# Optimization experiments

Hardware: AMD Instinct MI355X
Metric: run time of the kernel (lower is better)

The kernel has to match this reference:

```python
import jax, jax.numpy as jnp
import numpy as np

T, B, H, OUT = 64, 4096, 256, 2
SLOPE = 25.0  # snntorch surrogate.fast_sigmoid default slope


@jax.custom_vjp
def spike(x):
    # Heaviside forward, fast-sigmoid surrogate gradient backward
    return (x > 0).astype(x.dtype)

def _spk_fwd(x):
    return (x > 0).astype(x.dtype), x

def _spk_bwd(x, g):
    return (g / (SLOPE * jnp.abs(x) + 1.0) ** 2,)

spike.defvjp(_spk_fwd, _spk_bwd)


def temporal_embedding(length):
    center = length // 2
    sigma = length / 10
    pos = np.arange(length)
    e = np.exp(-0.5 * ((pos - center) / sigma) ** 2)
    e = (e - e.min()) / (e.max() - e.min())
    return jnp.asarray(e, dtype=jnp.float32)


def setup_inputs() -> dict:
    key = jax.random.key(0)
    ks = jax.random.split(key, 16)

    def lin(k, o, i):
        bound = 1.0 / np.sqrt(i)
        kw, kb = jax.random.split(k)
        W = jax.random.uniform(kw, (o, i), minval=-bound, maxval=bound, dtype=jnp.float32)
        b = jax.random.uniform(kb, (o,), minval=-bound, maxval=bound, dtype=jnp.float32)
        return W, b

    W_in, b_in = lin(ks[0], H, 3)
    W_h, b_h = lin(ks[1], H, H)
    W_h2, b_h2 = lin(ks[2], H, H)
    W_out, b_out = lin(ks[3], OUT, H)
    W_pred, b_pred = lin(ks[4], OUT, T * 4)
    u = lambda k, n: jax.random.uniform(k, (n,), dtype=jnp.float32)
    return {
        "x": jax.random.normal(ks[5], (T, B, 3), dtype=jnp.float32),
        "W_in": W_in, "b_in": b_in,
        "beta_in": u(ks[6], H), "thr_in": u(ks[7], H),
        "W_h": W_h, "b_h": b_h,
        "beta_h": u(ks[8], H), "thr_h": u(ks[9], H),
        "W_h2": W_h2, "b_h2": b_h2,
        "beta_h2": u(ks[10], H), "thr_h2": u(ks[11], H),
        "W_out": W_out, "b_out": b_out,
        "beta_out": u(ks[12], OUT),
        "W_pred": W_pred, "b_pred": b_pred,
    }


def reference(x, W_in, b_in, beta_in, thr_in, W_h, b_h, beta_h, thr_h,
              W_h2, b_h2, beta_h2, thr_h2, W_out, b_out, beta_out,
              W_pred, b_pred):
    Tn, Bsz = x.shape[0], x.shape[1]
    emb = temporal_embedding(Tn)
    x = x * emb[:, None, None]  # per-timestep Gaussian temporal weighting

    def lif(cur, mem, beta, thr):
        # snnTorch Leaky, reset_mechanism='subtract': reset from PREVIOUS mem (detached)
        reset = jax.lax.stop_gradient((mem - thr > 0).astype(cur.dtype))
        mem = jnp.clip(beta, 0.0, 1.0) * mem + cur - reset * thr
        return spike(mem - thr), mem

    def step(carry, x_t):
        m1, m2, m4, m3 = carry
        s1, m1 = lif(x_t @ W_in.T + b_in, m1, beta_in, thr_in)
        s2, m2 = lif(s1 @ W_h.T + b_h, m2, beta_h, thr_h)
        s4, m4 = lif(s2 @ W_h2.T + b_h2, m4, beta_h2, thr_h2)
        # li_out: reset_mechanism='none', default threshold=1.0
        m3 = jnp.clip(beta_out, 0.0, 1.0) * m3 + s4 @ W_out.T + b_out
        spk_out = spike(m3 - 1.0)
        return (m1, m2, m4, m3), (spk_out, m3)

    z = lambda n: jnp.zeros((Bsz, n), x.dtype)
    init = (z(W_in.shape[0]), z(W_h.shape[0]), z(W_h2.shape[0]), z(W_out.shape[0]))
    _, (spk_rec, mem_rec) = jax.lax.scan(step, init, x)
    out = jnp.concatenate([spk_rec, mem_rec], axis=-1)  # [T, B, 2*OUT]
    # torch .view(B, T*2*OUT) on contiguous [T,B,2*OUT] == plain reshape
    out = out.reshape(Bsz, Tn * out.shape[-1])
    return out @ W_pred.T + b_pred  # [B, OUT]
```

## Files before the change

kernel.cpp:

```cpp
#include <hip/hip_runtime.h>
#include <hip/hip_bf16.h>

#define TT 64
#define BB 4096
#define HH 256
#define BMb 16
#define NBLK (BB / BMb)
#define TC 4
#define NCH (TT / TC)

typedef short bf16x8_t __attribute__((ext_vector_type(8)));
typedef float f32x4_t  __attribute__((ext_vector_type(4)));

#define WS_WA_B   0u
#define WS_EMB_B  786432u
#define WS_REC_B  1048576u

__device__ __forceinline__ float clip01f(float v) {
    return fminf(fmaxf(v, 0.0f), 1.0f);
}

__global__ __launch_bounds__(64) void setup_emb_kernel(float* __restrict__ emb) {
    int i = threadIdx.x;
    const double sigma = 64.0 / 10.0;
    const double c = 32.0;
    double d = ((double)i - c) / sigma;
    double e = exp(-0.5 * (d * d));
    double d0 = (0.0 - c) / sigma;
    double emin = exp(-0.5 * (d0 * d0));
    emb[i] = (float)((e - emin) / (1.0 - emin));
}

__global__ __launch_bounds__(256) void split_weights_kernel(
    const float* __restrict__ W_h, const float* __restrict__ W_h2,
    unsigned short* __restrict__ WA)
{
    int flat = blockIdx.x * 256 + threadIdx.x;
    int j     = flat & 7;
    int lane  = (flat >> 3) & 63;
    int c     = flat >> 9;
    int tile  = c & 1;
    int c2    = c >> 1;
    int part  = c2 % 3;
    int c3    = c2 / 3;
    int kt    = c3 & 7;
    int c4    = c3 >> 3;
    int layer = c4 & 1;
    int wv    = c4 >> 1;
    int ntile = wv * 2 + tile;
    int k = kt * 32 + (lane >> 4) * 8 + j;
    int n = ntile * 16 + (lane & 15);
    const float* W = layer ? W_h2 : W_h;
    float w = W[n * HH + k];
    __hip_bfloat16 h = __float2bfloat16(w);
    float r1 = w - __bfloat162float(h);
    __hip_bfloat16 m = __float2bfloat16(r1);
    float r2 = r1 - __bfloat162float(m);
    __hip_bfloat16 l = __float2bfloat16(r2);
    __hip_bfloat16 v = (part == 0) ? h : ((part == 1) ? m : l);
    WA[flat] = *reinterpret_cast<unsigned short*>(&v);
}

union U16x8 { uint4 u; bf16x8_t v; };


#define AS1 __attribute__((address_space(1)))
#define AS3 __attribute__((address_space(3)))
__device__ __forceinline__ void gl16(const void* g, void* l) {
    __builtin_amdgcn_global_load_lds((AS1 const void*)g, (AS3 void*)l, 16, 0, 0);
}

#define ISSUE6(Wc, ktn, sl) do {                                               \
    const char* gb_ = (const char*)(Wc) + (ktn) * 6144;                        \
    char* lb_ = myring + (sl) * 6144;                                          \
    gl16(gb_,          lb_);                                                   \
    gl16(gb_ + 1024,   lb_ + 1024);                                            \
    gl16(gb_ + 2048,   lb_ + 2048);                                            \
    gl16(gb_ + 3072,   lb_ + 3072);                                            \
    gl16(gb_ + 4096,   lb_ + 4096);                                            \
    gl16(gb_ + 5120,   lb_ + 5120);                                            \
} while (0)

#define MFMA8T(wa_, wb_, ktb) do {                                             \
    _Pragma("unroll")                                                          \
    for (int tt_ = 0; tt_ < TC; ++tt_) {                                       \
        U16x8 br_; br_.u = BfL[tt_ * 512 + (ktb) * 64];                        \
        D0[tt_] = __builtin_amdgcn_mfma_f32_16x16x32_bf16(wa_.v, br_.v, D0[tt_], 0, 0, 0); \
        D1[tt_] = __builtin_amdgcn_mfma_f32_16x16x32_bf16(wb_.v, br_.v, D1[tt_], 0, 0, 0); \
    }                                                                          \
} while (0)

#define STEPT(sl, ktb, Wi, kti) do {                                           \
    asm volatile("s_waitcnt vmcnt(6)" ::: "memory");                           \
    __builtin_amdgcn_sched_barrier(0);                                         \
    {                                                                          \
        U16x8 wa_, wb_;                                                        \
        wa_.u = ringRd[(sl) * 384 + 0];                                        \
        wb_.u = ringRd[(sl) * 384 + 64];                                       \
        MFMA8T(wa_, wb_, ktb);                                                 \
    }                                                                          \
    {                                                                          \
        U16x8 wa_, wb_;                                                        \
        wa_.u = ringRd[(sl) * 384 + 128];                                      \
        wb_.u = ringRd[(sl) * 384 + 192];                                      \
        MFMA8T(wa_, wb_, ktb);                                                 \
    }                                                                          \
    {                                                                          \
        U16x8 wa_, wb_;                                                        \
        wa_.u = ringRd[(sl) * 384 + 256];                                      \
        wb_.u = ringRd[(sl) * 384 + 320];                                      \
        asm volatile("s_waitcnt lgkmcnt(0)" ::: "memory");                     \
        __builtin_amdgcn_sched_barrier(0);                                     \
        ISSUE6(Wi, kti, sl);                                                   \
        MFMA8T(wa_, wb_, ktb);                                                 \
    }                                                                          \
} while (0)

#define GPHASE(Wc, Wn) do {                                                    \
    STEPT(0, 0, Wc, 2);                                                        \
    STEPT(1, 1, Wc, 3);                                                        \
    STEPT(0, 2, Wc, 4);                                                        \
    STEPT(1, 3, Wc, 5);                                                        \
    STEPT(0, 4, Wc, 6);                                                        \
    STEPT(1, 5, Wc, 7);                                                        \
    STEPT(0, 6, Wn, 0);                                                        \
    STEPT(1, 7, Wn, 1);                                                        \
} while (0)

__device__ __forceinline__ void compute_p(
    const float* __restrict__ WoutS, const unsigned long long (*__restrict__ M3Lt)[4],
    int wb, int ooc, float* __restrict__ pout, int lane)
{
    if (lane < 32) {
        float p = 0.f;
        for (int k = 0; k < HH; ++k) {
            int ww = k >> 4, gg = (k >> 2) & 3, reg = k & 3;
            unsigned long long word = M3Lt[ww][reg];
            unsigned w32 = (gg < 2) ? (unsigned)word : (unsigned)(word >> 32);
            int sh = ((gg & 1) << 4) | wb;
            unsigned bit = (w32 >> sh) & 1u;
            float wv = WoutS[ooc * HH + k];
            p = p + (bit ? wv : 0.f);
        }
        pout[lane] = p;
    }
}

__device__ __forceinline__ void li_walker_bits(
    const float* __restrict__ WoutS, const unsigned long long (*__restrict__ M3Lt)[4],
    int wb, int ooc, float bto, float bo, float& m3s,
    float* __restrict__ rec, int t, int b0, int lane)
{
    if (lane < 32) {
        float p = 0.f;
        for (int k = 0; k < HH; ++k) {
            int ww = k >> 4, gg = (k >> 2) & 3, reg = k & 3;
            unsigned long long word = M3Lt[ww][reg];
            unsigned w32 = (gg < 2) ? (unsigned)word : (unsigned)(word >> 32);
            int sh = ((gg & 1) << 4) | wb;
            unsigned bit = (w32 >> sh) & 1u;
            float wv = WoutS[ooc * HH + k];
            p = p + (bit ? wv : 0.f);
        }
        float mm3 = fmaf(bto, m3s, p);
        mm3 = mm3 + bo;
        m3s = mm3;
        float spk = ((m3s - 1.0f) > 0.f) ? 1.f : 0.f;
        float om3 = __shfl_xor(m3s, 16, 64);
        float osp = __shfl_xor(spk, 16, 64);
        if (lane < 16) {
            *(float4*)(rec + ((size_t)t * BB + b0 + wb) * 4) =
                make_float4(spk, osp, m3s, om3);
        }
    }
}

__global__ __launch_bounds__(512) void snn_main_kernel(
    const float* __restrict__ x,
    const float* __restrict__ W_in, const float* __restrict__ b_in,
    const float* __restrict__ beta_in, const float* __restrict__ thr_in,
    const float* __restrict__ b_h, const float* __restrict__ beta_h, const float* __restrict__ thr_h,
    const float* __restrict__ b_h2, const float* __restrict__ beta_h2, const float* __restrict__ thr_h2,
    const float* __restrict__ W_out, const float* __restrict__ b_out, const float* __restrict__ beta_out,
    const unsigned short* __restrict__ WA, const float* __restrict__ emb,
    float* __restrict__ rec)
{
#pragma clang fp contract(off)
    const int tid = threadIdx.x;
    const int w = tid >> 6;
    const int lane = tid & 63;
    const int b = lane & 15;
    const int g = lane >> 4;
    const int b0 = blockIdx.x * BMb;

    __shared__ __align__(16) unsigned short frag[TC][8 * 64 * 8];
    __shared__ unsigned long long M3L[TC][16][4];
    __shared__ float pbuf[TC][32];
    __shared__ __align__(16) float WoutS[2 * HH];
    __shared__ float4 PL1a[HH];
    __shared__ float2 PL1b[HH];
    __shared__ float4 PL2[HH];
    __shared__ float4 PL3[HH];
    __shared__ float  xs[TT][BMb][3];
    __shared__ float  embS[TT];
    __shared__ __align__(16) char ring[8 * 2 * 6144];

    char* myring = ring + w * 12288;
    const uint4* ringRd = (const uint4*)(ring + w * 12288 + lane * 16);
    const uint4* BfL = (const uint4*)frag + lane;

    WoutS[tid] = W_out[tid];
    if (tid < HH) {
        int n = tid;
        PL1a[n] = make_float4(W_in[n * 3], W_in[n * 3 + 1], W_in[n * 3 + 2], b_in[n]);
        PL1b[n] = make_float2(clip01f(beta_in[n]), thr_in[n]);
        PL2[n]  = make_float4(b_h[n],  clip01f(beta_h[n]),  thr_h[n],  0.f);
        PL3[n]  = make_float4(b_h2[n], clip01f(beta_h2[n]), thr_h2[n], 0.f);
    }
    if (tid < TT) embS[tid] = emb[tid];
#pragma unroll
    for (int i = tid; i < TT * BMb; i += 512) {
        int ts = i >> 4, bb = i & 15;
        const float* xp = x + ((size_t)ts * BB + b0 + bb) * 3;
        xs[ts][bb][0] = xp[0];
        xs[ts][bb][1] = xp[1];
        xs[ts][bb][2] = xp[2];
    }

    const int nb0 = w * 32 + g * 4;

    float m1[2][4], m2[2][4], m4[2][4];
#pragma unroll
    for (int u = 0; u < 2; ++u)
#pragma unroll
        for (int r = 0; r < 4; ++r) { m1[u][r] = 0.f; m2[u][r] = 0.f; m4[u][r] = 0.f; }

    const int sb0 = ((w * 64 + ((g >> 1) * 16 + b)) * 8 + (g & 1) * 4);

    const int wb = lane & 15;
    const int ooc = (lane >> 4) & 1;
    float bto = clip01f(beta_out[ooc]);
    float bo = b_out[ooc];
    float m3s = 0.f;

    const uint4* W2 = (const uint4*)WA + (size_t)w * 6144 + lane;
    const uint4* W3 = W2 + 3072;

    ISSUE6(W2, 0, 0);
    ISSUE6(W2, 1, 1);

    __syncthreads();

#pragma unroll 1
    for (int c = 0; c < NCH; ++c) {
        const int t0 = c * TC;

#pragma unroll
        for (int tt = 0; tt < TC; ++tt) {
            const int t = t0 + tt;
            float et = embS[t];
            float xe0 = xs[t][b][0] * et;
            float xe1 = xs[t][b][1] * et;
            float xe2 = xs[t][b][2] * et;
            unsigned sp[2][4];
#pragma unroll
            for (int u = 0; u < 2; ++u)
#pragma unroll
            for (int r = 0; r < 4; ++r) {
                int n = nb0 + u * 16 + r;
                float4 pa = PL1a[n];
                float2 pb = PL1b[n];
                float a1 = xe0 * pa.x;
                a1 = fmaf(xe1, pa.y, a1);
                a1 = fmaf(xe2, pa.z, a1);
                float cur = a1 + pa.w;
                float rf = ((m1[u][r] - pb.y) > 0.f) ? 1.f : 0.f;
                float mm = fmaf(pb.x, m1[u][r], cur);
                mm = fmaf(-rf, pb.y, mm);
                m1[u][r] = mm;
                sp[u][r] = ((mm - pb.y) > 0.f) ? 0x3F80u : 0u;
            }
            *(uint2*)(&frag[tt][sb0])       = make_uint2(sp[0][0] | (sp[0][1] << 16), sp[0][2] | (sp[0][3] << 16));
            *(uint2*)(&frag[tt][sb0 + 256]) = make_uint2(sp[1][0] | (sp[1][1] << 16), sp[1][2] | (sp[1][3] << 16));
        }
        __syncthreads();

        if (w < TC && c > 0)
            compute_p(WoutS, M3L[w], wb, ooc, pbuf[w], lane);

        f32x4_t D0[TC], D1[TC];
#pragma unroll
        for (int tt = 0; tt < TC; ++tt) {
            D0[tt] = (f32x4_t){0.f, 0.f, 0.f, 0.f};
            D1[tt] = (f32x4_t){0.f, 0.f, 0.f, 0.f};
        }
        GPHASE(W2, W3);

        uint2 s2w[TC][2];
#pragma unroll
        for (int tt = 0; tt < TC; ++tt) {
            unsigned sp[2][4];
#pragma unroll
            for (int r = 0; r < 4; ++r) {
                int n0 = nb0 + r;
                float4 p2 = PL2[n0];
                float cur = D0[tt][r] + p2.x;
                float rf = ((m2[0][r] - p2.z) > 0.f) ? 1.f : 0.f;
                float mm = fmaf(p2.y, m2[0][r], cur);
                mm = fmaf(-rf, p2.z, mm);
                m2[0][r] = mm;
                sp[0][r] = ((mm - p2.z) > 0.f) ? 0x3F80u : 0u;
            }
#pragma unroll
            for (int r = 0; r < 4; ++r) {
                int n1 = nb0 + 16 + r;
                float4 p2 = PL2[n1];
                float cur = D1[tt][r] + p2.x;
                float rf = ((m2[1][r] - p2.z) > 0.f) ? 1.f : 0.f;
                float mm = fmaf(p2.y, m2[1][r], cur);
                mm = fmaf(-rf, p2.z, mm);
                m2[1][r] = mm;
                sp[1][r] = ((mm - p2.z) > 0.f) ? 0x3F80u : 0u;
            }
            s2w[tt][0] = make_uint2(sp[0][0] | (sp[0][1] << 16), sp[0][2] | (sp[0][3] << 16));
            s2w[tt][1] = make_uint2(sp[1][0] | (sp[1][1] << 16), sp[1][2] | (sp[1][3] << 16));
        }
        __syncthreads();

        if (w == 0 && c > 0 && lane < 32) {
#pragma unroll
            for (int tt = 0; tt < TC; ++tt) {
                float p = pbuf[tt][lane];
                float mm3 = fmaf(bto, m3s, p);
                mm3 = mm3 + bo;
                m3s = mm3;
                float spk = ((m3s - 1.0f) > 0.f) ? 1.f : 0.f;
                float om3 = __shfl_xor(m3s, 16, 64);
                float osp = __shfl_xor(spk, 16, 64);
                if (lane < 16) {
                    *(float4*)(rec + ((size_t)(t0 - TC + tt) * BB + b0 + wb) * 4) =
                        make_float4(spk, osp, m3s, om3);
                }
            }
        }

#pragma unroll
        for (int tt = 0; tt < TC; ++tt) {
            *(uint2*)(&frag[tt][sb0])       = s2w[tt][0];
            *(uint2*)(&frag[tt][sb0 + 256]) = s2w[tt][1];
        }
        __syncthreads();

#pragma unroll
        for (int tt = 0; tt < TC; ++tt) {
            D0[tt] = (f32x4_t){0.f, 0.f, 0.f, 0.f};
            D1[tt] = (f32x4_t){0.f, 0.f, 0.f, 0.f};
        }
        GPHASE(W3, W2);

#pragma unroll
        for (int tt = 0; tt < TC; ++tt) {
#pragma unroll
            for (int u = 0; u < 2; ++u) {
#pragma unroll
                for (int r = 0; r < 4; ++r) {
                    int n = nb0 + u * 16 + r;
                    float4 p3 = PL3[n];
                    float cur = ((u == 0) ? D0[tt][r] : D1[tt][r]) + p3.x;
                    float rf = ((m4[u][r] - p3.z) > 0.f) ? 1.f : 0.f;
                    float mm = fmaf(p3.y, m4[u][r], cur);
                    mm = fmaf(-rf, p3.z, mm);
                    m4[u][r] = mm;
                    bool s3 = (mm - p3.z) > 0.f;
                    unsigned long long mk = __ballot(s3);
                    if (lane == 0) M3L[tt][2 * w + u][r] = mk;
                }
            }
        }
        __syncthreads();
    }

    if (w == 0) {
#pragma unroll
        for (int tt = 0; tt < TC; ++tt)
            li_walker_bits(WoutS, M3L[tt], wb, ooc, bto, bo, m3s,
                           rec, TT - TC + tt, b0, lane);
    }
}

__global__ __launch_bounds__(256) void pred_kernel(
    const float* __restrict__ rec, const float* __restrict__ W_pred,
    const float* __restrict__ b_pred, float* __restrict__ out)
{
#pragma clang fp contract(off)
    int r = blockIdx.x * 256 + threadIdx.x;
    const float* f = rec + (size_t)r * 256;
    float a0 = 0.f, a1 = 0.f;
#pragma unroll 4
    for (int c = 0; c < 256; ++c) {
        float v = f[c];
        a0 = fmaf(v, W_pred[c], a0);
        a1 = fmaf(v, W_pred[256 + c], a1);
    }
    out[r * 2 + 0] = a0 + b_pred[0];
    out[r * 2 + 1] = a1 + b_pred[1];
}

extern "C" void kernel_launch(void* const* d_in, const int* in_sizes, int n_in,
                              void* d_out, int out_size, void* d_ws, size_t ws_size,
                              hipStream_t stream)
{
    const float* x        = (const float*)d_in[0];
    const float* W_in     = (const float*)d_in[1];
    const float* b_in     = (const float*)d_in[2];
    const float* beta_in  = (const float*)d_in[3];
    const float* thr_in   = (const float*)d_in[4];
    const float* W_h      = (const float*)d_in[5];
    const float* b_h      = (const float*)d_in[6];
    const float* beta_h   = (const float*)d_in[7];
    const float* thr_h    = (const float*)d_in[8];
    const float* W_h2     = (const float*)d_in[9];
    const float* b_h2     = (const float*)d_in[10];
    const float* beta_h2  = (const float*)d_in[11];
    const float* thr_h2   = (const float*)d_in[12];
    const float* W_out    = (const float*)d_in[13];
    const float* b_out    = (const float*)d_in[14];
    const float* beta_out = (const float*)d_in[15];
    const float* W_pred   = (const float*)d_in[16];
    const float* b_pred   = (const float*)d_in[17];

    char* ws = (char*)d_ws;
    unsigned short* WA = (unsigned short*)(ws + WS_WA_B);
    float* emb = (float*)(ws + WS_EMB_B);
    float* rec = (float*)(ws + WS_REC_B);

    split_weights_kernel<<<1536, 256, 0, stream>>>(W_h, W_h2, WA);
    setup_emb_kernel<<<1, 64, 0, stream>>>(emb);

    snn_main_kernel<<<NBLK, 512, 0, stream>>>(
        x, W_in, b_in, beta_in, thr_in,
        b_h, beta_h, thr_h,
        b_h2, beta_h2, thr_h2,
        W_out, b_out, beta_out,
        WA, emb, rec);

    pred_kernel<<<BB / 256, 256, 0, stream>>>(rec, W_pred, b_pred, (float*)d_out);
}
```

Baseline: 652.9 us.

## Halve main-kernel block to 4 waves, each covering two neuron halves

The main SNN kernel now runs with 256 threads (4 waves) instead of 512, and each wave processes two 128-neuron halves per layer, so there are twice as many GEMM phases chained through the weight ring. Layer-2 spikes now go through per-wave ballot masks in shared memory, which every wave decodes to rebuild the bf16 fragment. The ring buffer is halved, cutting shared memory per block so more blocks may fit per CU. The trade-off is more serial work and more register state per wave, plus extra ballot and decode steps.

```diff
diff --git a/kernel.cpp b/kernel.cpp
--- a/kernel.cpp
+++ b/kernel.cpp
@@ -175,7 +175,7 @@
     }
 }
 
-__global__ __launch_bounds__(512) void snn_main_kernel(
+__global__ __launch_bounds__(256) void snn_main_kernel(
     const float* __restrict__ x,
     const float* __restrict__ W_in, const float* __restrict__ b_in,
     const float* __restrict__ beta_in, const float* __restrict__ thr_in,
@@ -195,6 +195,7 @@
 
     __shared__ __align__(16) unsigned short frag[TC][8 * 64 * 8];
     __shared__ unsigned long long M3L[TC][16][4];
+    __shared__ unsigned long long S2M[TC][16][4];
     __shared__ float pbuf[TC][32];
     __shared__ __align__(16) float WoutS[2 * HH];
     __shared__ float4 PL1a[HH];
@@ -203,14 +204,15 @@
     __shared__ float4 PL3[HH];
     __shared__ float  xs[TT][BMb][3];
     __shared__ float  embS[TT];
-    __shared__ __align__(16) char ring[8 * 2 * 6144];
+    __shared__ __align__(16) char ring[4 * 2 * 6144];
 
     char* myring = ring + w * 12288;
     const uint4* ringRd = (const uint4*)(ring + w * 12288 + lane * 16);
     const uint4* BfL = (const uint4*)frag + lane;
 
-    WoutS[tid] = W_out[tid];
-    if (tid < HH) {
+#pragma unroll
+    for (int i = tid; i < 2 * HH; i += 256) WoutS[i] = W_out[i];
+    {
         int n = tid;
         PL1a[n] = make_float4(W_in[n * 3], W_in[n * 3 + 1], W_in[n * 3 + 2], b_in[n]);
         PL1b[n] = make_float2(clip01f(beta_in[n]), thr_in[n]);
@@ -219,7 +221,7 @@
     }
     if (tid < TT) embS[tid] = emb[tid];
 #pragma unroll
-    for (int i = tid; i < TT * BMb; i += 512) {
+    for (int i = tid; i < TT * BMb; i += 256) {
         int ts = i >> 4, bb = i & 15;
         const float* xp = x + ((size_t)ts * BB + b0 + bb) * 3;
         xs[ts][bb][0] = xp[0];
@@ -229,9 +231,9 @@
 
     const int nb0 = w * 32 + g * 4;
 
-    float m1[2][4], m2[2][4], m4[2][4];
-#pragma unroll
-    for (int u = 0; u < 2; ++u)
+    float m1[4][4], m2[4][4], m4[4][4];
+#pragma unroll
+    for (int u = 0; u < 4; ++u)
 #pragma unroll
         for (int r = 0; r < 4; ++r) { m1[u][r] = 0.f; m2[u][r] = 0.f; m4[u][r] = 0.f; }
 
@@ -243,11 +245,14 @@
     float bo = b_out[ooc];
     float m3s = 0.f;
 
-    const uint4* W2 = (const uint4*)WA + (size_t)w * 6144 + lane;
-    const uint4* W3 = W2 + 3072;
-
-    ISSUE6(W2, 0, 0);
-    ISSUE6(W2, 1, 1);
+    const uint4* WAu4 = (const uint4*)WA;
+    const uint4* W2h0 = WAu4 + (size_t)w * 6144 + lane;
+    const uint4* W2h1 = WAu4 + (size_t)(w + 4) * 6144 + lane;
+    const uint4* W3h0 = W2h0 + 3072;
+    const uint4* W3h1 = W2h1 + 3072;
+
+    ISSUE6(W2h0, 0, 0);
+    ISSUE6(W2h0, 1, 1);
 
     __syncthreads();
 
@@ -262,12 +267,12 @@
             float xe0 = xs[t][b][0] * et;
             float xe1 = xs[t][b][1] * et;
             float xe2 = xs[t][b][2] * et;
-            unsigned sp[2][4];
-#pragma unroll
-            for (int u = 0; u < 2; ++u)
+            unsigned sp[4][4];
+#pragma unroll
+            for (int u = 0; u < 4; ++u)
 #pragma unroll
             for (int r = 0; r < 4; ++r) {
-                int n = nb0 + u * 16 + r;
+                int n = nb0 + (u & 1) * 16 + (u >> 1) * 128 + r;
                 float4 pa = PL1a[n];
                 float2 pb = PL1b[n];
                 float a1 = xe0 * pa.x;
@@ -280,50 +285,68 @@
                 m1[u][r] = mm;
                 sp[u][r] = ((mm - pb.y) > 0.f) ? 0x3F80u : 0u;
             }
-            *(uint2*)(&frag[tt][sb0])       = make_uint2(sp[0][0] | (sp[0][1] << 16), sp[0][2] | (sp[0][3] << 16));
-            *(uint2*)(&frag[tt][sb0 + 256]) = make_uint2(sp[1][0] | (sp[1][1] << 16), sp[1][2] | (sp[1][3] << 16));
+            *(uint2*)(&frag[tt][sb0])        = make_uint2(sp[0][0] | (sp[0][1] << 16), sp[0][2] | (sp[0][3] << 16));
+            *(uint2*)(&frag[tt][sb0 + 256])  = make_uint2(sp[1][0] | (sp[1][1] << 16), sp[1][2] | (sp[1][3] << 16));
+            *(uint2*)(&frag[tt][sb0 + 2048]) = make_uint2(sp[2][0] | (sp[2][1] << 16), sp[2][2] | (sp[2][3] << 16));
+            *(uint2*)(&frag[tt][sb0 + 2304]) = make_uint2(sp[3][0] | (sp[3][1] << 16), sp[3][2] | (sp[3][3] << 16));
         }
         __syncthreads();
 
-        if (w < TC && c > 0)
+        if (c > 0)
             compute_p(WoutS, M3L[w], wb, ooc, pbuf[w], lane);
 
         f32x4_t D0[TC], D1[TC];
+
 #pragma unroll
         for (int tt = 0; tt < TC; ++tt) {
             D0[tt] = (f32x4_t){0.f, 0.f, 0.f, 0.f};
             D1[tt] = (f32x4_t){0.f, 0.f, 0.f, 0.f};
         }
-        GPHASE(W2, W3);
-
-        uint2 s2w[TC][2];
-#pragma unroll
-        for (int tt = 0; tt < TC; ++tt) {
-            unsigned sp[2][4];
-#pragma unroll
-            for (int r = 0; r < 4; ++r) {
-                int n0 = nb0 + r;
-                float4 p2 = PL2[n0];
-                float cur = D0[tt][r] + p2.x;
-                float rf = ((m2[0][r] - p2.z) > 0.f) ? 1.f : 0.f;
-                float mm = fmaf(p2.y, m2[0][r], cur);
-                mm = fmaf(-rf, p2.z, mm);
-                m2[0][r] = mm;
-                sp[0][r] = ((mm - p2.z) > 0.f) ? 0x3F80u : 0u;
-            }
-#pragma unroll
-            for (int r = 0; r < 4; ++r) {
-                int n1 = nb0 + 16 + r;
-                float4 p2 = PL2[n1];
-                float cur = D1[tt][r] + p2.x;
-                float rf = ((m2[1][r] - p2.z) > 0.f) ? 1.f : 0.f;
-                float mm = fmaf(p2.y, m2[1][r], cur);
-                mm = fmaf(-rf, p2.z, mm);
-                m2[1][r] = mm;
-                sp[1][r] = ((mm - p2.z) > 0.f) ? 0x3F80u : 0u;
-            }
-            s2w[tt][0] = make_uint2(sp[0][0] | (sp[0][1] << 16), sp[0][2] | (sp[0][3] << 16));
-            s2w[tt][1] = make_uint2(sp[1][0] | (sp[1][1] << 16), sp[1][2] | (sp[1][3] << 16));
+        GPHASE(W2h0, W2h1);
+#pragma unroll
+        for (int tt = 0; tt < TC; ++tt) {
+#pragma unroll
+            for (int u = 0; u < 2; ++u) {
+#pragma unroll
+                for (int r = 0; r < 4; ++r) {
+                    int n = nb0 + u * 16 + r;
+                    float4 p2 = PL2[n];
+                    float cur = ((u == 0) ? D0[tt][r] : D1[tt][r]) + p2.x;
+                    float rf = ((m2[u][r] - p2.z) > 0.f) ? 1.f : 0.f;
+                    float mm = fmaf(p2.y, m2[u][r], cur);
+                    mm = fmaf(-rf, p2.z, mm);
+                    m2[u][r] = mm;
+                    bool s2 = (mm - p2.z) > 0.f;
+                    unsigned long long mk = __ballot(s2);
+                    if (lane == 0) S2M[tt][2 * w + u][r] = mk;
+                }
+            }
+        }
+
+#pragma unroll
+        for (int tt = 0; tt < TC; ++tt) {
+            D0[tt] = (f32x4_t){0.f, 0.f, 0.f, 0.f};
+            D1[tt] = (f32x4_t){0.f, 0.f, 0.f, 0.f};
+        }
+        GPHASE(W2h1, W3h0);
+#pragma unroll
+        for (int tt = 0; tt < TC; ++tt) {
+#pragma unroll
+            for (int v = 0; v < 2; ++v) {
+#pragma unroll
+                for (int r = 0; r < 4; ++r) {
+                    int n = nb0 + 128 + v * 16 + r;
+                    float4 p2 = PL2[n];
+                    float cur = ((v == 0) ? D0[tt][r] : D1[tt][r]) + p2.x;
+                    float rf = ((m2[2 + v][r] - p2.z) > 0.f) ? 1.f : 0.f;
+                    float mm = fmaf(p2.y, m2[2 + v][r], cur);
+                    mm = fmaf(-rf, p2.z, mm);
+                    m2[2 + v][r] = mm;
+                    bool s2 = (mm - p2.z) > 0.f;
+                    unsigned long long mk = __ballot(s2);
+                    if (lane == 0) S2M[tt][8 + 2 * w + v][r] = mk;
+                }
+            }
         }
         __syncthreads();
 
@@ -346,8 +369,25 @@
 
 #pragma unroll
         for (int tt = 0; tt < TC; ++tt) {
-            *(uint2*)(&frag[tt][sb0])       = s2w[tt][0];
-            *(uint2*)(&frag[tt][sb0 + 256]) = s2w[tt][1];
+            unsigned sp[4][4];
+#pragma unroll
+            for (int u = 0; u < 2; ++u)
+#pragma unroll
+            for (int r = 0; r < 4; ++r) {
+                unsigned long long mk = S2M[tt][2 * w + u][r];
+                sp[u][r] = ((mk >> lane) & 1ull) ? 0x3F80u : 0u;
+            }
+#pragma unroll
+            for (int v = 0; v < 2; ++v)
+#pragma unroll
+            for (int r = 0; r < 4; ++r) {
+                unsigned long long mk = S2M[tt][8 + 2 * w + v][r];
+                sp[2 + v][r] = ((mk >> lane) & 1ull) ? 0x3F80u : 0u;
+            }
+            *(uint2*)(&frag[tt][sb0])        = make_uint2(sp[0][0] | (sp[0][1] << 16), sp[0][2] | (sp[0][3] << 16));
+            *(uint2*)(&frag[tt][sb0 + 256])  = make_uint2(sp[1][0] | (sp[1][1] << 16), sp[1][2] | (sp[1][3] << 16));
+            *(uint2*)(&frag[tt][sb0 + 2048]) = make_uint2(sp[2][0] | (sp[2][1] << 16), sp[2][2] | (sp[2][3] << 16));
+            *(uint2*)(&frag[tt][sb0 + 2304]) = make_uint2(sp[3][0] | (sp[3][1] << 16), sp[3][2] | (sp[3][3] << 16));
         }
         __syncthreads();
 
@@ -356,8 +396,7 @@
             D0[tt] = (f32x4_t){0.f, 0.f, 0.f, 0.f};
             D1[tt] = (f32x4_t){0.f, 0.f, 0.f, 0.f};
         }
-        GPHASE(W3, W2);
-
+        GPHASE(W3h0, W3h1);
 #pragma unroll
         for (int tt = 0; tt < TC; ++tt) {
 #pragma unroll
@@ -374,6 +413,32 @@
                     bool s3 = (mm - p3.z) > 0.f;
                     unsigned long long mk = __ballot(s3);
                     if (lane == 0) M3L[tt][2 * w + u][r] = mk;
+                }
+            }
+        }
+
+#pragma unroll
+        for (int tt = 0; tt < TC; ++tt) {
+            D0[tt] = (f32x4_t){0.f, 0.f, 0.f, 0.f};
+            D1[tt] = (f32x4_t){0.f, 0.f, 0.f, 0.f};
+        }
+        GPHASE(W3h1, W2h0);
+#pragma unroll
+        for (int tt = 0; tt < TC; ++tt) {
+#pragma unroll
+            for (int v = 0; v < 2; ++v) {
+#pragma unroll
+                for (int r = 0; r < 4; ++r) {
+                    int n = nb0 + 128 + v * 16 + r;
+                    float4 p3 = PL3[n];
+                    float cur = ((v == 0) ? D0[tt][r] : D1[tt][r]) + p3.x;
+                    float rf = ((m4[2 + v][r] - p3.z) > 0.f) ? 1.f : 0.f;
+                    float mm = fmaf(p3.y, m4[2 + v][r], cur);
+                    mm = fmaf(-rf, p3.z, mm);
+                    m4[2 + v][r] = mm;
+                    bool s3 = (mm - p3.z) > 0.f;
+                    unsigned long long mk = __ballot(s3);
+                    if (lane == 0) M3L[tt][8 + 2 * w + v][r] = mk;
                 }
             }
         }
@@ -437,7 +502,7 @@
     split_weights_kernel<<<1536, 256, 0, stream>>>(W_h, W_h2, WA);
     setup_emb_kernel<<<1, 64, 0, stream>>>(emb);
 
-    snn_main_kernel<<<NBLK, 512, 0, stream>>>(
+    snn_main_kernel<<<NBLK, 256, 0, stream>>>(
         x, W_in, b_in, beta_in, thr_in,
         b_h, beta_h, thr_h,
         b_h2, beta_h2, thr_h2,
```

After: 674.5 us. 3.3% more time.

## Split each hidden-layer GEMM into two half-N passes with a smaller weight ring

Applied to the files above, without the earlier changes.

Each wave now computes one 16-column N tile per pass instead of two, running two sequential GPHASE passes per layer over the two halves of the output columns. The per-wave LDS weight ring and the per-step async load batch are halved, and the weight pre-split layout is reordered to match. Layer-2 spikes are now passed through ballot masks in a new shared S2M buffer rather than held in registers across the barrier. This cuts register and LDS pressure, which could raise occupancy, but it doubles the number of pipeline phases and leaves fewer independent MFMA chains in flight per wave.

```diff
diff --git a/kernel.cpp b/kernel.cpp
--- a/kernel.cpp
+++ b/kernel.cpp
@@ -39,15 +39,12 @@
     int j     = flat & 7;
     int lane  = (flat >> 3) & 63;
     int c     = flat >> 9;
-    int tile  = c & 1;
-    int c2    = c >> 1;
-    int part  = c2 % 3;
-    int c3    = c2 / 3;
+    int part  = c % 3;
+    int c3    = c / 3;
     int kt    = c3 & 7;
     int c4    = c3 >> 3;
     int layer = c4 & 1;
-    int wv    = c4 >> 1;
-    int ntile = wv * 2 + tile;
+    int ntile = c4 >> 1;
     int k = kt * 32 + (lane >> 4) * 8 + j;
     int n = ntile * 16 + (lane & 15);
     const float* W = layer ? W_h2 : W_h;
@@ -70,49 +67,39 @@
     __builtin_amdgcn_global_load_lds((AS1 const void*)g, (AS3 void*)l, 16, 0, 0);
 }
 
-#define ISSUE6(Wc, ktn, sl) do {                                               \
-    const char* gb_ = (const char*)(Wc) + (ktn) * 6144;                        \
-    char* lb_ = myring + (sl) * 6144;                                          \
+#define ISSUE3(Wc, ktn, sl) do {                                               \
+    const char* gb_ = (const char*)(Wc) + (ktn) * 3072;                        \
+    char* lb_ = myring + (sl) * 3072;                                          \
     gl16(gb_,          lb_);                                                   \
     gl16(gb_ + 1024,   lb_ + 1024);                                            \
     gl16(gb_ + 2048,   lb_ + 2048);                                            \
-    gl16(gb_ + 3072,   lb_ + 3072);                                            \
-    gl16(gb_ + 4096,   lb_ + 4096);                                            \
-    gl16(gb_ + 5120,   lb_ + 5120);                                            \
 } while (0)
 
-#define MFMA8T(wa_, wb_, ktb) do {                                             \
+#define MFMA4T(wa_, ktb) do {                                                  \
     _Pragma("unroll")                                                          \
     for (int tt_ = 0; tt_ < TC; ++tt_) {                                       \
         U16x8 br_; br_.u = BfL[tt_ * 512 + (ktb) * 64];                        \
-        D0[tt_] = __builtin_amdgcn_mfma_f32_16x16x32_bf16(wa_.v, br_.v, D0[tt_], 0, 0, 0); \
-        D1[tt_] = __builtin_amdgcn_mfma_f32_16x16x32_bf16(wb_.v, br_.v, D1[tt_], 0, 0, 0); \
+        D[tt_] = __builtin_amdgcn_mfma_f32_16x16x32_bf16(wa_.v, br_.v, D[tt_], 0, 0, 0); \
     }                                                                          \
 } while (0)
 
 #define STEPT(sl, ktb, Wi, kti) do {                                           \
-    asm volatile("s_waitcnt vmcnt(6)" ::: "memory");                           \
+    asm volatile("s_waitcnt vmcnt(3)" ::: "memory");                           \
     __builtin_amdgcn_sched_barrier(0);                                         \
     {                                                                          \
-        U16x8 wa_, wb_;                                                        \
-        wa_.u = ringRd[(sl) * 384 + 0];                                        \
-        wb_.u = ringRd[(sl) * 384 + 64];                                       \
-        MFMA8T(wa_, wb_, ktb);                                                 \
+        U16x8 wa_; wa_.u = ringRd[(sl) * 192 + 0];                             \
+        MFMA4T(wa_, ktb);                                                      \
     }                                                                          \
     {                                                                          \
-        U16x8 wa_, wb_;                                                        \
-        wa_.u = ringRd[(sl) * 384 + 128];                                      \
-        wb_.u = ringRd[(sl) * 384 + 192];                                      \
-        MFMA8T(wa_, wb_, ktb);                                                 \
+        U16x8 wa_; wa_.u = ringRd[(sl) * 192 + 64];                            \
+        MFMA4T(wa_, ktb);                                                      \
     }                                                                          \
     {                                                                          \
-        U16x8 wa_, wb_;                                                        \
-        wa_.u = ringRd[(sl) * 384 + 256];                                      \
-        wb_.u = ringRd[(sl) * 384 + 320];                                      \
+        U16x8 wa_; wa_.u = ringRd[(sl) * 192 + 128];                           \
         asm volatile("s_waitcnt lgkmcnt(0)" ::: "memory");                     \
         __builtin_amdgcn_sched_barrier(0);                                     \
-        ISSUE6(Wi, kti, sl);                                                   \
-        MFMA8T(wa_, wb_, ktb);                                                 \
+        ISSUE3(Wi, kti, sl);                                                   \
+        MFMA4T(wa_, ktb);                                                      \
     }                                                                          \
 } while (0)
 
@@ -195,6 +182,7 @@
 
     __shared__ __align__(16) unsigned short frag[TC][8 * 64 * 8];
     __shared__ unsigned long long M3L[TC][16][4];
+    __shared__ unsigned long long S2M[TC][16][4];
     __shared__ float pbuf[TC][32];
     __shared__ __align__(16) float WoutS[2 * HH];
     __shared__ float4 PL1a[HH];
@@ -203,10 +191,10 @@
     __shared__ float4 PL3[HH];
     __shared__ float  xs[TT][BMb][3];
     __shared__ float  embS[TT];
-    __shared__ __align__(16) char ring[8 * 2 * 6144];
-
-    char* myring = ring + w * 12288;
-    const uint4* ringRd = (const uint4*)(ring + w * 12288 + lane * 16);
+    __shared__ __align__(16) char ring[8 * 2 * 3072];
+
+    char* myring = ring + w * 6144;
+    const uint4* ringRd = (const uint4*)(ring + w * 6144 + lane * 16);
     const uint4* BfL = (const uint4*)frag + lane;
 
     WoutS[tid] = W_out[tid];
@@ -227,7 +215,7 @@
         xs[ts][bb][2] = xp[2];
     }
 
-    const int nb0 = w * 32 + g * 4;
+    const int nb0 = w * 16 + g * 4;
 
     float m1[2][4], m2[2][4], m4[2][4];
 #pragma unroll
@@ -235,7 +223,7 @@
 #pragma unroll
         for (int r = 0; r < 4; ++r) { m1[u][r] = 0.f; m2[u][r] = 0.f; m4[u][r] = 0.f; }
 
-    const int sb0 = ((w * 64 + ((g >> 1) * 16 + b)) * 8 + (g & 1) * 4);
+    const int sb0 = (((w >> 1) * 64 + (((w & 1) * 2 + (g >> 1)) * 16 + b)) * 8 + (g & 1) * 4);
 
     const int wb = lane & 15;
     const int ooc = (lane >> 4) & 1;
@@ -243,11 +231,14 @@
     float bo = b_out[ooc];
     float m3s = 0.f;
 
-    const uint4* W2 = (const uint4*)WA + (size_t)w * 6144 + lane;
-    const uint4* W3 = W2 + 3072;
-
-    ISSUE6(W2, 0, 0);
-    ISSUE6(W2, 1, 1);
+    const uint4* WAu4 = (const uint4*)WA;
+    const uint4* W2h0 = WAu4 + (size_t)w * 3072 + lane;
+    const uint4* W2h1 = WAu4 + (size_t)(8 + w) * 3072 + lane;
+    const uint4* W3h0 = W2h0 + 1536;
+    const uint4* W3h1 = W2h1 + 1536;
+
+    ISSUE3(W2h0, 0, 0);
+    ISSUE3(W2h0, 1, 1);
 
     __syncthreads();
 
@@ -267,7 +258,7 @@
             for (int u = 0; u < 2; ++u)
 #pragma unroll
             for (int r = 0; r < 4; ++r) {
-                int n = nb0 + u * 16 + r;
+                int n = nb0 + u * 128 + r;
                 float4 pa = PL1a[n];
                 float2 pb = PL1b[n];
                 float a1 = xe0 * pa.x;
@@ -280,50 +271,54 @@
                 m1[u][r] = mm;
                 sp[u][r] = ((mm - pb.y) > 0.f) ? 0x3F80u : 0u;
             }
-            *(uint2*)(&frag[tt][sb0])       = make_uint2(sp[0][0] | (sp[0][1] << 16), sp[0][2] | (sp[0][3] << 16));
-            *(uint2*)(&frag[tt][sb0 + 256]) = make_uint2(sp[1][0] | (sp[1][1] << 16), sp[1][2] | (sp[1][3] << 16));
+            *(uint2*)(&frag[tt][sb0])        = make_uint2(sp[0][0] | (sp[0][1] << 16), sp[0][2] | (sp[0][3] << 16));
+            *(uint2*)(&frag[tt][sb0 + 2048]) = make_uint2(sp[1][0] | (sp[1][1] << 16), sp[1][2] | (sp[1][3] << 16));
         }
         __syncthreads();
 
         if (w < TC && c > 0)
             compute_p(WoutS, M3L[w], wb, ooc, pbuf[w], lane);
 
-        f32x4_t D0[TC], D1[TC];
-#pragma unroll
-        for (int tt = 0; tt < TC; ++tt) {
-            D0[tt] = (f32x4_t){0.f, 0.f, 0.f, 0.f};
-            D1[tt] = (f32x4_t){0.f, 0.f, 0.f, 0.f};
-        }
-        GPHASE(W2, W3);
-
-        uint2 s2w[TC][2];
-#pragma unroll
-        for (int tt = 0; tt < TC; ++tt) {
-            unsigned sp[2][4];
-#pragma unroll
-            for (int r = 0; r < 4; ++r) {
-                int n0 = nb0 + r;
-                float4 p2 = PL2[n0];
-                float cur = D0[tt][r] + p2.x;
+        f32x4_t D[TC];
+
+#pragma unroll
+        for (int tt = 0; tt < TC; ++tt) D[tt] = (f32x4_t){0.f, 0.f, 0.f, 0.f};
+        GPHASE(W2h0, W2h1);
+#pragma unroll
+        for (int tt = 0; tt < TC; ++tt) {
+#pragma unroll
+            for (int r = 0; r < 4; ++r) {
+                int n = nb0 + r;
+                float4 p2 = PL2[n];
+                float cur = D[tt][r] + p2.x;
                 float rf = ((m2[0][r] - p2.z) > 0.f) ? 1.f : 0.f;
                 float mm = fmaf(p2.y, m2[0][r], cur);
                 mm = fmaf(-rf, p2.z, mm);
                 m2[0][r] = mm;
-                sp[0][r] = ((mm - p2.z) > 0.f) ? 0x3F80u : 0u;
-            }
-#pragma unroll
-            for (int r = 0; r < 4; ++r) {
-                int n1 = nb0 + 16 + r;
-                float4 p2 = PL2[n1];
-                float cur = D1[tt][r] + p2.x;
+                bool s2 = (mm - p2.z) > 0.f;
+                unsigned long long mk = __ballot(s2);
+                if (lane == 0) S2M[tt][w][r] = mk;
+            }
+        }
+
+#pragma unroll
+        for (int tt = 0; tt < TC; ++tt) D[tt] = (f32x4_t){0.f, 0.f, 0.f, 0.f};
+        GPHASE(W2h1, W3h0);
+#pragma unroll
+        for (int tt = 0; tt < TC; ++tt) {
+#pragma unroll
+            for (int r = 0; r < 4; ++r) {
+                int n = nb0 + 128 + r;
+                float4 p2 = PL2[n];
+                float cur = D[tt][r] + p2.x;
                 float rf = ((m2[1][r] - p2.z) > 0.f) ? 1.f : 0.f;
                 float mm = fmaf(p2.y, m2[1][r], cur);
                 mm = fmaf(-rf, p2.z, mm);
                 m2[1][r] = mm;
-                sp[1][r] = ((mm - p2.z) > 0.f) ? 0x3F80u : 0u;
-            }
-            s2w[tt][0] = make_uint2(sp[0][0] | (sp[0][1] << 16), sp[0][2] | (sp[0][3] << 16));
-            s2w[tt][1] = make_uint2(sp[1][0] | (sp[1][1] << 16), sp[1][2] | (sp[1][3] << 16));
+                bool s2 = (mm - p2.z) > 0.f;
+                unsigned long long mk = __ballot(s2);
+                if (lane == 0) S2M[tt][8 + w][r] = mk;
+            }
         }
         __syncthreads();
 
@@ -346,35 +341,56 @@
 
 #pragma unroll
         for (int tt = 0; tt < TC; ++tt) {
-            *(uint2*)(&frag[tt][sb0])       = s2w[tt][0];
-            *(uint2*)(&frag[tt][sb0 + 256]) = s2w[tt][1];
+            unsigned sp[2][4];
+#pragma unroll
+            for (int u = 0; u < 2; ++u)
+#pragma unroll
+            for (int r = 0; r < 4; ++r) {
+                unsigned long long mk = S2M[tt][w + 8 * u][r];
+                sp[u][r] = ((mk >> lane) & 1ull) ? 0x3F80u : 0u;
+            }
+            *(uint2*)(&frag[tt][sb0])        = make_uint2(sp[0][0] | (sp[0][1] << 16), sp[0][2] | (sp[0][3] << 16));
+            *(uint2*)(&frag[tt][sb0 + 2048]) = make_uint2(sp[1][0] | (sp[1][1] << 16), sp[1][2] | (sp[1][3] << 16));
         }
         __syncthreads();
 
 #pragma unroll
-        for (int tt = 0; tt < TC; ++tt) {
-            D0[tt] = (f32x4_t){0.f, 0.f, 0.f, 0.f};
-            D1[tt] = (f32x4_t){0.f, 0.f, 0.f, 0.f};
-        }
-        GPHASE(W3, W2);
-
-#pragma unroll
-        for (int tt = 0; tt < TC; ++tt) {
-#pragma unroll
-            for (int u = 0; u < 2; ++u) {
-#pragma unroll
-                for (int r = 0; r < 4; ++r) {
-                    int n = nb0 + u * 16 + r;
-                    float4 p3 = PL3[n];
-                    float cur = ((u == 0) ? D0[tt][r] : D1[tt][r]) + p3.x;
-                    float rf = ((m4[u][r] - p3.z) > 0.f) ? 1.f : 0.f;
-                    float mm = fmaf(p3.y, m4[u][r], cur);
-                    mm = fmaf(-rf, p3.z, mm);
-                    m4[u][r] = mm;
-                    bool s3 = (mm - p3.z) > 0.f;
-                    unsigned long long mk = __ballot(s3);
-                    if (lane == 0) M3L[tt][2 * w + u][r] = mk;
-                }
+        for (int tt = 0; tt < TC; ++tt) D[tt] = (f32x4_t){0.f, 0.f, 0.f, 0.f};
+        GPHASE(W3h0, W3h1);
+#pragma unroll
+        for (int tt = 0; tt < TC; ++tt) {
+#pragma unroll
+            for (int r = 0; r < 4; ++r) {
+                int n = nb0 + r;
+                float4 p3 = PL3[n];
+                float cur = D[tt][r] + p3.x;
+                float rf = ((m4[0][r] - p3.z) > 0.f) ? 1.f : 0.f;
+                float mm = fmaf(p3.y, m4[0][r], cur);
+                mm = fmaf(-rf, p3.z, mm);
+                m4[0][r] = mm;
+                bool s3 = (mm - p3.z) > 0.f;
+                unsigned long long mk = __ballot(s3);
+                if (lane == 0) M3L[tt][w][r] = mk;
+            }
+        }
+
+#pragma unroll
+        for (int tt = 0; tt < TC; ++tt) D[tt] = (f32x4_t){0.f, 0.f, 0.f, 0.f};
+        GPHASE(W3h1, W2h0);
+#pragma unroll
+        for (int tt = 0; tt < TC; ++tt) {
+#pragma unroll
+            for (int r = 0; r < 4; ++r) {
+                int n = nb0 + 128 + r;
+                float4 p3 = PL3[n];
+                float cur = D[tt][r] + p3.x;
+                float rf = ((m4[1][r] - p3.z) > 0.f) ? 1.f : 0.f;
+                float mm = fmaf(p3.y, m4[1][r], cur);
+                mm = fmaf(-rf, p3.z, mm);
+                m4[1][r] = mm;
+                bool s3 = (mm - p3.z) > 0.f;
+                unsigned long long mk = __ballot(s3);
+                if (lane == 0) M3L[tt][8 + w][r] = mk;
             }
         }
         __syncthreads();
```

Result: no change. 653.4 us (+0.1%).
